# Kernel optimization log

Measured on AMD Instinct MI355X. Metric: run time of the kernel, lower is better.

## Reference

```python
import jax, jax.numpy as jnp
import numpy as np

# ---- forest structure (static) ----
B = 32                      # number of trees in the batch
DEPTH = 12                  # topological levels per tree
LEVELS = [2 ** d for d in range(DEPTH)]           # nodes per level (root=level 0)
STARTS = np.concatenate([[0], np.cumsum(LEVELS)[:-1]]).astype(int)
NPG = int(sum(LEVELS))      # 4095 nodes per graph, node 0 = root
N = B * NPG                 # 131040 total nodes
VOCAB = 20000               # dataset.PAD_TOKEN_VALUE + 1
PAD = VOCAB - 1             # padding_idx
E = 256                     # embedding_dim (x_size)
H = 256                     # lstm_output_dim (h_size)
C = 104                     # num_classes (extra_non_linear=None)


def setup_inputs() -> dict:
    key = jax.random.key(0)
    ks = jax.random.split(key, 8)
    # random parent in the previous level for every non-root node (irregular fan-in)
    rng = np.random.RandomState(0)
    par = np.full(N, -1, dtype=np.int64)
    for g in range(B):
        off = g * NPG
        for d in range(1, DEPTH):
            nd = LEVELS[d]
            par[off + STARTS[d]: off + STARTS[d] + nd] = (
                off + STARTS[d - 1] + rng.randint(0, LEVELS[d - 1], size=nd))
    s = 0.05
    return {
        'x': jax.random.randint(ks[0], (N,), 0, VOCAB),
        'par': jnp.asarray(par),
        'emb': jax.random.normal(ks[1], (VOCAB, E), jnp.float32) * s,
        'W_iou': jax.random.normal(ks[2], (3 * H, E), jnp.float32) * s,
        'U_iou': jax.random.normal(ks[3], (3 * H, H), jnp.float32) * s,
        'b_iou': jnp.zeros((1, 3 * H), jnp.float32),
        'U_f_w': jax.random.normal(ks[4], (H, H), jnp.float32) * s,
        'U_f_b': jnp.zeros((H,), jnp.float32),
        'lin_w': jax.random.normal(ks[5], (C, H), jnp.float32) * s,
        'lin_b': jnp.zeros((C,), jnp.float32),
    }


def _forward(x, par, emb, W_iou, U_iou, b_iou, U_f_w, U_f_b, lin_w, lin_b):
    emb = emb.at[PAD].set(0.0)                 # padding_idx row is zero
    x_vec = emb[x]                             # [N, E]
    iou = x_vec @ W_iou.T                      # [N, 3H], W_iou has no bias
    h = jnp.zeros((N, H), x_vec.dtype)
    c = jnp.zeros((N, H), x_vec.dtype)
    offs = jnp.arange(B) * NPG
    # topological propagation: leaves (deepest level) -> root, per generation
    for d in range(DEPTH - 1, -1, -1):
        nd = LEVELS[d]
        nids = (offs[:, None] + STARTS[d] + jnp.arange(nd)).reshape(-1)  # [B*nd]
        iou_n = iou[nids]
        if d < DEPTH - 1:
            nc = LEVELS[d + 1]
            cids = (offs[:, None] + STARTS[d + 1] + jnp.arange(nc)).reshape(-1)
            h_ch = h[cids]                     # mailbox gather of child states
            c_ch = c[cids]
            p = par[cids]                      # global parent id per child
            seg = (p // NPG) * nd + (p % NPG - STARTS[d])  # parent slot in this level
            f = jax.nn.sigmoid(h_ch @ U_f_w.T + U_f_b)     # per-child forget gate
            h_tild = jax.ops.segment_sum(h_ch, seg, num_segments=B * nd)
            c_agg = jax.ops.segment_sum(f * c_ch, seg, num_segments=B * nd)
            iou_n = iou_n + h_tild @ U_iou.T
            c_n = c_agg
        else:
            c_n = jnp.zeros((B * nd, H), x_vec.dtype)
        iou_n = iou_n + b_iou
        i, o, u = jnp.split(iou_n, 3, axis=1)
        c_new = jax.nn.sigmoid(i) * jnp.tanh(u) + c_n
        h_new = jax.nn.sigmoid(o) * jnp.tanh(c_new)
        h = h.at[nids].set(h_new)
        c = c.at[nids].set(c_new)
    roots = h[offs]                            # graph.ndata['h'][0] per graph
    return roots @ lin_w.T + lin_b             # [B, num_classes]


def reference(x, par, emb, W_iou, U_iou, b_iou, U_f_w, U_f_b, lin_w, lin_b):
    return _forward(x, par, emb, W_iou, U_iou, b_iou, U_f_w, U_f_b, lin_w, lin_b)
```

## Files before the change

### kernel.cpp

```cpp
#include <hip/hip_runtime.h>
#include <hip/hip_bf16.h>


#define B_G     32
#define NPG     4095
#define NTOT    (B_G * NPG)
#define NCLS    104
#define VOCAB   20000
#define PAD_TOK 19999
#define KCAP    24
#define LB(d)   (32 * ((1 << (d)) - 1))

#define EMB_BLKS  2500
#define WUC_BLKS  1536
#define UFC_BLKS  256
#define PREP_BLKS 512
#define CONV_BLKS (EMB_BLKS + WUC_BLKS + UFC_BLKS + PREP_BLKS)

typedef unsigned short u16;
typedef unsigned int   u32;
typedef __attribute__((ext_vector_type(8))) short bfrag8;
typedef __attribute__((ext_vector_type(4))) float ffrag4;

__device__ __forceinline__ float bf2f(u16 v) {
    union { u32 u; float f; } x; x.u = ((u32)v) << 16; return x.f;
}
__device__ __forceinline__ u16 f2bf(float f) {
    union { __hip_bfloat16 h; u16 u; } c; c.h = __float2bfloat16(f); return c.u;
}
__device__ __forceinline__ float loadv(const void* b, int i, int isf32) {
    return isf32 ? ((const float*)b)[i] : bf2f(((const u16*)b)[i]);
}
__device__ __forceinline__ float sigf(float x) { return 1.f / (1.f + __expf(-x)); }

__global__ __launch_bounds__(384) void probe_kernel(
    const void* emb, const void* Wiou, const void* Uiou,
    const void* Ufw, const void* lw,
    const int* x32, const int* par32, int* flags)
{
    if (blockIdx.x != 0) return;
    const int w = threadIdx.x >> 6, lane = threadIdx.x & 63;
    const void* ptrs[5] = { emb, Wiou, Uiou, Ufw, lw };
    if (w < 5) {
        const u16* p = (const u16*)ptrs[w];
        int big = 0;
        #pragma unroll
        for (int k = 0; k < 2; ++k) {
            u32 e = (((u32)p[lane * 2 + k]) << 16 >> 23) & 0xFF;
            if (e >= 129) ++big;
        }
        unsigned long long m1 = __ballot(big >= 1);
        unsigned long long m2 = __ballot(big >= 2);
        int tot = __popcll(m1) + __popcll(m2);
        if (lane == 0) flags[w] = (tot >= 4) ? 1 : 0;
    } else if (w == 5) {
        int bad = (lane < 8) ? (x32[2 * lane + 1] != 0) : 0;
        unsigned long long mx = __ballot(bad != 0);
        if (lane == 0) {
            flags[5] = (mx == 0) ? 1 : 0;
            flags[6] = (par32[3] == 0 && par32[5] == 0) ? 1 : 0;
        }
    }
}

__global__ __launch_bounds__(256) void convert_kernel(
    const void* __restrict__ emb, u16* __restrict__ embb,
    const void* __restrict__ Wiou, const void* __restrict__ Uiou,
    u16* __restrict__ wuc,
    const void* __restrict__ Ufw, u16* __restrict__ ufc,
    const int* __restrict__ x, const int* __restrict__ par,
    int* __restrict__ tokLvl, int* __restrict__ cnt, int* __restrict__ bucket,
    const int* __restrict__ flags)
{
    const int b = blockIdx.x;
    if (b < EMB_BLKS) {
        int i8 = (b * 256 + (int)threadIdx.x) * 8;
        if (i8 >= VOCAB * 256) return;
        u16 v[8];
        if ((i8 >> 8) == PAD_TOK) {
            #pragma unroll
            for (int s = 0; s < 8; ++s) v[s] = 0;
        } else if (flags[0]) {
            const float* e = (const float*)emb + i8;
            float4 a = *(const float4*)e;
            float4 c = *(const float4*)(e + 4);
            v[0]=f2bf(a.x); v[1]=f2bf(a.y); v[2]=f2bf(a.z); v[3]=f2bf(a.w);
            v[4]=f2bf(c.x); v[5]=f2bf(c.y); v[6]=f2bf(c.z); v[7]=f2bf(c.w);
        } else {
            *(uint4*)v = *(const uint4*)((const u16*)emb + i8);
        }
        *(uint4*)(embb + i8) = *(uint4*)v;
    } else if (b < EMB_BLKS + WUC_BLKS) {
        int idx = (b - EMB_BLKS) * 256 + (int)threadIdx.x;
        if (idx >= 16 * 768 * 32) return;
        int c   = idx / 24576;
        int rem = idx - c * 24576;
        int out = rem >> 5;
        int kk  = rem & 31;
        int k   = c * 32 + kk;
        float v = (k < 256) ? loadv(Wiou, out * 256 + k, flags[1])
                            : loadv(Uiou, out * 256 + (k - 256), flags[2]);
        wuc[idx] = f2bf(v);
    } else if (b < EMB_BLKS + WUC_BLKS + UFC_BLKS) {
        int idx = (b - EMB_BLKS - WUC_BLKS) * 256 + (int)threadIdx.x;
        if (idx >= 8 * 256 * 32) return;
        int c   = idx >> 13;
        int rem = idx & 8191;
        int out = rem >> 5;
        int kk  = rem & 31;
        ufc[idx] = f2bf(loadv(Ufw, out * 256 + c * 32 + kk, flags[3]));
    } else {
        int gid = (b - EMB_BLKS - WUC_BLKS - UFC_BLKS) * 256 + (int)threadIdx.x;
        if (gid >= NTOT) return;
        int g     = (int)((u32)gid / NPG);
        int local = gid - g * NPG;
        int v  = local + 1;
        int d  = 31 - __clz(v);
        int j  = local - ((1 << d) - 1);
        int tok = flags[5] ? x[2 * gid] : x[gid];
        if (tok < 0 || tok >= VOCAB) tok = PAD_TOK;
        tokLvl[LB(d) + (g << d) + j] = tok;
        if (local > 0) {
            int p  = flags[6] ? par[2 * gid] : par[gid];
            p = max(0, min(p, NTOT - 1));
            int pg = (int)((u32)p / NPG);
            int pl = p - pg * NPG;
            int pd = d - 1;
            int ps = LB(pd) + (pg << pd) + (pl - ((1 << pd) - 1));
            ps = max(0, min(ps, 65503));
            int slot = atomicAdd(&cnt[ps], 1);
            if (slot < KCAP) bucket[(size_t)ps * KCAP + slot] = (g << d) + j;
        }
    }
}

__global__ __launch_bounds__(256, 3) void gemm1_kernel(
    const u16* __restrict__ hch, u16* cbuf,
    const u16* __restrict__ ufc, const void* __restrict__ ufb,
    const int* __restrict__ flags)
{
    __shared__ union {
        struct { u16 As[64][40]; u16 Bs[256][40]; } k;
        u16 tile[64][264];
    } sm;
    auto& As = sm.k.As;
    auto& Bs = sm.k.Bs;
    auto& tile = sm.tile;
    const int t = threadIdx.x;
    const int w = t >> 6, lane = t & 63, quad = lane >> 4, l15 = lane & 15;
    const int m0 = blockIdx.x * 64;
    const int f_uf = flags[3];

    ffrag4 acc[4][4];
    #pragma unroll
    for (int i = 0; i < 4; ++i)
        #pragma unroll
        for (int j = 0; j < 4; ++j) acc[i][j] = (ffrag4)0.f;

    const int arow = t >> 2, aseg = t & 3;
    for (int c = 0; c < 8; ++c) {
        *(uint4*)&As[arow][aseg * 8] =
            *(const uint4*)(hch + (size_t)(m0 + arow) * 256 + c * 32 + aseg * 8);
        #pragma unroll
        for (int r16 = 0; r16 < 4; ++r16) {
            int row = r16 * 64 + arow;
            *(uint4*)&Bs[row][aseg * 8] =
                *(const uint4*)(ufc + ((size_t)c * 256 + row) * 32 + aseg * 8);
        }
        __syncthreads();
        bfrag8 a[4], b[4];
        #pragma unroll
        for (int mt = 0; mt < 4; ++mt) a[mt] = *(bfrag8*)&As[mt * 16 + l15][quad * 8];
        #pragma unroll
        for (int nt = 0; nt < 4; ++nt) b[nt] = *(bfrag8*)&Bs[w * 64 + nt * 16 + l15][quad * 8];
        #pragma unroll
        for (int mt = 0; mt < 4; ++mt)
            #pragma unroll
            for (int nt = 0; nt < 4; ++nt)
                acc[mt][nt] = __builtin_amdgcn_mfma_f32_16x16x32_bf16(a[mt], b[nt], acc[mt][nt], 0, 0, 0);
        __syncthreads();
    }

    const int srow = t >> 2, sseg = t & 3;
    const size_t sgb = (size_t)(m0 + srow) * 256 + sseg * 64;
    #pragma unroll
    for (int k = 0; k < 8; ++k)
        *(uint4*)&tile[srow][sseg * 64 + k * 8] = *(const uint4*)(cbuf + sgb + k * 8);
    __syncthreads();

    #pragma unroll
    for (int nt = 0; nt < 4; ++nt) {
        int hu = w * 64 + nt * 16 + l15;
        float fb = loadv(ufb, hu, f_uf);
        #pragma unroll
        for (int mt = 0; mt < 4; ++mt) {
            #pragma unroll
            for (int r = 0; r < 4; ++r) {
                int row = mt * 16 + quad * 4 + r;
                float f = sigf(acc[mt][nt][r] + fb);
                tile[row][hu] = f2bf(f * bf2f(tile[row][hu]));
            }
        }
    }
    __syncthreads();
    #pragma unroll
    for (int k = 0; k < 8; ++k)
        *(uint4*)(cbuf + sgb + k * 8) = *(const uint4*)&tile[srow][sseg * 64 + k * 8];
}

__global__ __launch_bounds__(256) void agg_kernel(
    int NN, const u32* __restrict__ hch32, const u32* __restrict__ fcch32,
    const int* __restrict__ cnt_d, const int* __restrict__ bucket_d,
    u32* __restrict__ htild32, u32* __restrict__ cagg32)
{
    int pi  = blockIdx.x * 2 + (threadIdx.x >> 7);
    int col = threadIdx.x & 127;
    if (pi >= NN) return;
    int nc = min(cnt_d[pi], KCAP);
    float h0 = 0.f, h1 = 0.f, c0 = 0.f, c1 = 0.f;
    for (int ci = 0; ci < nc; ++ci) {
        int ch = bucket_d[(size_t)pi * KCAP + ci];
        u32 hv = hch32[(size_t)ch * 128 + col];
        u32 fv = fcch32[(size_t)ch * 128 + col];
        h0 += bf2f((u16)(hv & 0xffff)); h1 += bf2f((u16)(hv >> 16));
        c0 += bf2f((u16)(fv & 0xffff)); c1 += bf2f((u16)(fv >> 16));
    }
    htild32[(size_t)pi * 128 + col] = (u32)f2bf(h0) | ((u32)f2bf(h1) << 16);
    cagg32[(size_t)pi * 128 + col]  = (u32)f2bf(c0) | ((u32)f2bf(c1) << 16);
}

__global__ __launch_bounds__(256, 3) void gemm2_kernel(
    int nchunk, int NN,
    const int* __restrict__ tokLvl_d, const u16* __restrict__ embb,
    const u16* __restrict__ wuc, const void* __restrict__ biou,
    const u16* __restrict__ htild, const u16* __restrict__ cagg,
    u16* __restrict__ hdst, u16* __restrict__ cdst,
    const int* __restrict__ flags)
{
    __shared__ union {
        struct { u16 As[128][40]; u16 Bs[192][40]; } k;
        u16 tile[128][72];
    } sm;
    __shared__ int toks[128];
    auto& As = sm.k.As;
    auto& Bs = sm.k.Bs;
    auto& tile = sm.tile;
    const int t = threadIdx.x;
    const int w = t >> 6, lane = t & 63, quad = lane >> 4, l15 = lane & 15;
    const int m0 = blockIdx.x * 128;
    const int q  = blockIdx.y;
    const int f_b = flags[1];

    if (t < 128) toks[t] = tokLvl_d[m0 + t];
    __syncthreads();

    ffrag4 acc[8][3];
    #pragma unroll
    for (int i = 0; i < 8; ++i)
        #pragma unroll
        for (int j = 0; j < 3; ++j) acc[i][j] = (ffrag4)0.f;

    const int arow = t >> 1, ac0 = (t & 1) * 16;
    const int brow = t >> 2, bseg = t & 3;
    for (int c = 0; c < nchunk; ++c) {
        if (c < 8) {
            const u16* e = embb + (size_t)toks[arow] * 256 + c * 32 + ac0;
            *(uint4*)&As[arow][ac0]     = *(const uint4*)e;
            *(uint4*)&As[arow][ac0 + 8] = *(const uint4*)(e + 8);
        } else {
            const u16* hsrc = htild + (size_t)(m0 + arow) * 256 + (c - 8) * 32 + ac0;
            *(uint4*)&As[arow][ac0]     = *(const uint4*)hsrc;
            *(uint4*)&As[arow][ac0 + 8] = *(const uint4*)(hsrc + 8);
        }
        #pragma unroll
        for (int g = 0; g < 3; ++g) {
            *(uint4*)&Bs[g * 64 + brow][bseg * 8] =
                *(const uint4*)(wuc + ((size_t)c * 768 + g * 256 + q * 64 + brow) * 32 + bseg * 8);
        }
        __syncthreads();
        bfrag8 a[8], b[3];
        #pragma unroll
        for (int mt = 0; mt < 8; ++mt) a[mt] = *(bfrag8*)&As[mt * 16 + l15][quad * 8];
        #pragma unroll
        for (int g = 0; g < 3; ++g) b[g] = *(bfrag8*)&Bs[g * 64 + w * 16 + l15][quad * 8];
        #pragma unroll
        for (int mt = 0; mt < 8; ++mt)
            #pragma unroll
            for (int g = 0; g < 3; ++g)
                acc[mt][g] = __builtin_amdgcn_mfma_f32_16x16x32_bf16(a[mt], b[g], acc[mt][g], 0, 0, 0);
        __syncthreads();
    }

    const int hu  = q * 64 + w * 16 + l15;
    const int huL = w * 16 + l15;
    const float bi = loadv(biou, hu,       f_b);
    const float bo = loadv(biou, 256 + hu, f_b);
    const float bu = loadv(biou, 512 + hu, f_b);

    const int srow = t >> 1, sseg = t & 1;
    const size_t sgbase = (size_t)(m0 + srow) * 256 + q * 64 + sseg * 32;
    const bool svalid = (m0 + srow) < NN;

    if (cagg) {
        if (svalid) {
            #pragma unroll
            for (int k = 0; k < 4; ++k)
                *(uint4*)&tile[srow][sseg * 32 + k * 8] =
                    *(const uint4*)(cagg + sgbase + k * 8);
        }
    }
    __syncthreads();

    u16 cnv[8][4];
    #pragma unroll
    for (int mt = 0; mt < 8; ++mt) {
        #pragma unroll
        for (int r = 0; r < 4; ++r) {
            int row = mt * 16 + quad * 4 + r;
            float cg = cagg ? bf2f(tile[row][huL]) : 0.f;
            float iv = acc[mt][0][r] + bi;
            float ov = acc[mt][1][r] + bo;
            float uv = acc[mt][2][r] + bu;
            float cn = sigf(iv) * tanhf(uv) + cg;
            float hn = sigf(ov) * tanhf(cn);
            cnv[mt][r] = f2bf(cn);
            tile[row][huL] = f2bf(hn);
        }
    }
    __syncthreads();
    if (svalid) {
        #pragma unroll
        for (int k = 0; k < 4; ++k)
            *(uint4*)(hdst + sgbase + k * 8) = *(const uint4*)&tile[srow][sseg * 32 + k * 8];
    }
    __syncthreads();
    #pragma unroll
    for (int mt = 0; mt < 8; ++mt)
        #pragma unroll
        for (int r = 0; r < 4; ++r)
            tile[mt * 16 + quad * 4 + r][huL] = cnv[mt][r];
    __syncthreads();
    if (svalid) {
        #pragma unroll
        for (int k = 0; k < 4; ++k)
            *(uint4*)(cdst + sgbase + k * 8) = *(const uint4*)&tile[srow][sseg * 32 + k * 8];
    }
}

__global__ __launch_bounds__(1024, 1) void tail_kernel(
    const int* __restrict__ tokLvl, const u16* __restrict__ embb,
    const u16* __restrict__ wuc, const void* __restrict__ biou,
    const u16* __restrict__ ufc, const void* __restrict__ ufb,
    const u16* __restrict__ hB, const u16* __restrict__ cB,
    const int* __restrict__ cnt, const int* __restrict__ bucket,
    const void* __restrict__ lw, const void* __restrict__ lb,
    float* __restrict__ out, const int* __restrict__ flags)
{
    __shared__ u16 hs[64][264];
    __shared__ u16 cs[64][264];
    __shared__ u16 hts[32][264];
    __shared__ u16 cts[32][264];
    __shared__ float lred[8][NCLS];
    const int t = threadIdx.x;
    const int g = blockIdx.x;
    const int w = t >> 6;
    const int lane = t & 63, quad = lane >> 4, l15 = lane & 15;
    const int f_uf = flags[3], f_b = flags[1], f_lw = flags[4];

    #pragma unroll 1
    for (int i = t; i < 64 * 32; i += 1024) {
        int j = i >> 5, seg = i & 31;
        size_t off = (((size_t)((g << 6) + j)) << 8) + seg * 8;
        *(uint4*)&hs[j][seg * 8] = *(const uint4*)(hB + off);
        *(uint4*)&cs[j][seg * 8] = *(const uint4*)(cB + off);
    }
    __syncthreads();

    #pragma unroll 1
    for (int d = 5; d >= 0; --d) {
        const int ncr = 1 << (d + 1);
        const int np  = 1 << d;
        const int lvb = LB(d) + (g << d);
        const int hu  = w * 16 + l15;

        {
            ffrag4 facc[4];
            #pragma unroll
            for (int i = 0; i < 4; ++i) facc[i] = (ffrag4)0.f;
            #pragma unroll 4
            for (int c = 0; c < 8; ++c) {
                bfrag8 a[4];
                #pragma unroll
                for (int mt = 0; mt < 4; ++mt)
                    a[mt] = *(const bfrag8*)&hs[mt * 16 + l15][c * 32 + quad * 8];
                bfrag8 b = *(const bfrag8*)(ufc + ((size_t)c * 256 + w * 16 + l15) * 32 + quad * 8);
                #pragma unroll
                for (int mt = 0; mt < 4; ++mt)
                    facc[mt] = __builtin_amdgcn_mfma_f32_16x16x32_bf16(a[mt], b, facc[mt], 0, 0, 0);
            }
            float fb = loadv(ufb, hu, f_uf);
            #pragma unroll
            for (int mt = 0; mt < 4; ++mt) {
                #pragma unroll
                for (int r = 0; r < 4; ++r) {
                    int j = mt * 16 + quad * 4 + r;
                    if (j < ncr) {
                        float f = sigf(facc[mt][r] + fb);
                        cs[j][hu] = f2bf(f * bf2f(cs[j][hu]));
                    }
                }
            }
        }

        {
            const int pr = lane >> 3;
            const int colb = (w * 8 + (lane & 7)) * 2;
            #pragma unroll 1
            for (int pi = pr; pi < np; pi += 8) {
                int nc = min(cnt[lvb + pi], KCAP);
                const int* bk = bucket + (size_t)(lvb + pi) * KCAP;
                float h0 = 0.f, h1 = 0.f, c0 = 0.f, c1 = 0.f;
                #pragma unroll 1
                for (int ci = 0; ci < nc; ++ci) {
                    int j = bk[ci] & (ncr - 1);
                    u32 hv = *(const u32*)&hs[j][colb];
                    u32 cv = *(const u32*)&cs[j][colb];
                    h0 += bf2f((u16)(hv & 0xffff)); h1 += bf2f((u16)(hv >> 16));
                    c0 += bf2f((u16)(cv & 0xffff)); c1 += bf2f((u16)(cv >> 16));
                }
                *(u32*)&hts[pi][colb] = (u32)f2bf(h0) | ((u32)f2bf(h1) << 16);
                *(u32*)&cts[pi][colb] = (u32)f2bf(c0) | ((u32)f2bf(c1) << 16);
            }
        }
        __syncthreads();

        {
            int tok0 = tokLvl[lvb + min(l15, np - 1)];
            int tok1 = tokLvl[lvb + min(16 + l15, np - 1)];
            const u16* wb = wuc + ((size_t)w * 16 + l15) * 32 + quad * 8;
            ffrag4 acc[2][3];
            #pragma unroll
            for (int i = 0; i < 2; ++i)
                #pragma unroll
                for (int j = 0; j < 3; ++j) acc[i][j] = (ffrag4)0.f;
            #pragma unroll 4
            for (int c = 0; c < 8; ++c) {
                bfrag8 a0 = *(const bfrag8*)(embb + (size_t)tok0 * 256 + c * 32 + quad * 8);
                bfrag8 a1 = *(const bfrag8*)(embb + (size_t)tok1 * 256 + c * 32 + quad * 8);
                #pragma unroll
                for (int g3 = 0; g3 < 3; ++g3) {
                    bfrag8 b = *(const bfrag8*)(wb + ((size_t)c * 768 + g3 * 256) * 32);
                    acc[0][g3] = __builtin_amdgcn_mfma_f32_16x16x32_bf16(a0, b, acc[0][g3], 0, 0, 0);
                    acc[1][g3] = __builtin_amdgcn_mfma_f32_16x16x32_bf16(a1, b, acc[1][g3], 0, 0, 0);
                }
            }
            #pragma unroll 4
            for (int c8 = 0; c8 < 8; ++c8) {
                bfrag8 a0 = *(const bfrag8*)&hts[l15][c8 * 32 + quad * 8];
                bfrag8 a1 = *(const bfrag8*)&hts[16 + l15][c8 * 32 + quad * 8];
                #pragma unroll
                for (int g3 = 0; g3 < 3; ++g3) {
                    bfrag8 b = *(const bfrag8*)(wb + ((size_t)(c8 + 8) * 768 + g3 * 256) * 32);
                    acc[0][g3] = __builtin_amdgcn_mfma_f32_16x16x32_bf16(a0, b, acc[0][g3], 0, 0, 0);
                    acc[1][g3] = __builtin_amdgcn_mfma_f32_16x16x32_bf16(a1, b, acc[1][g3], 0, 0, 0);
                }
            }
            float bi = loadv(biou, hu,       f_b);
            float bo = loadv(biou, 256 + hu, f_b);
            float bu = loadv(biou, 512 + hu, f_b);
            #pragma unroll
            for (int mt = 0; mt < 2; ++mt) {
                #pragma unroll
                for (int r = 0; r < 4; ++r) {
                    int p = mt * 16 + quad * 4 + r;
                    if (p < np) {
                        float iv = acc[mt][0][r] + bi;
                        float ov = acc[mt][1][r] + bo;
                        float uv = acc[mt][2][r] + bu;
                        float cn = sigf(iv) * tanhf(uv) + bf2f(cts[p][hu]);
                        float hn = sigf(ov) * tanhf(cn);
                        hs[p][hu] = f2bf(hn);
                        cs[p][hu] = f2bf(cn);
                    }
                }
            }
        }
        __syncthreads();
    }

    {
        const int o  = t & 127;
        const int ks = t >> 7;
        if (o < NCLS) {
            float acc = 0.f;
            #pragma unroll 8
            for (int k = ks * 32; k < ks * 32 + 32; ++k)
                acc += loadv(lw, o * 256 + k, f_lw) * bf2f(hs[0][k]);
            lred[ks][o] = acc;
        }
        __syncthreads();
        if (t < NCLS) {
            float s = 0.f;
            #pragma unroll
            for (int i = 0; i < 8; ++i) s += lred[i][t];
            out[(size_t)g * NCLS + t] = s + loadv(lb, t, f_lw);
        }
    }
}

__global__ void fill_kernel(float* out, int n, float v) {
    int i = blockIdx.x * 256 + threadIdx.x;
    if (i < n) out[i] = v;
}

extern "C" void kernel_launch(void* const* d_in, const int* in_sizes, int n_in,
                              void* d_out, int out_size, void* d_ws, size_t ws_size,
                              hipStream_t stream)
{
    float* out = (float*)d_out;

    static const int exp_sizes[10] = {131040, 131040, 5120000, 196608, 196608,
                                      768, 65536, 256, 26624, 104};
    bool shapes_ok = (n_in == 10) && (out_size == B_G * NCLS);
    for (int i = 0; i < 10 && shapes_ok; ++i)
        if (in_sizes[i] != exp_sizes[i]) shapes_ok = false;
    if (!shapes_ok) {
        fill_kernel<<<(out_size + 255) / 256, 256, 0, stream>>>(out, out_size, 2.0f);
        return;
    }

    const int* x     = (const int*)d_in[0];
    const int* par   = (const int*)d_in[1];
    const void* emb  = d_in[2];
    const void* Wiou = d_in[3];
    const void* Uiou = d_in[4];
    const void* biou = d_in[5];
    const void* Ufw  = d_in[6];
    const void* Ufb  = d_in[7];
    const void* lw   = d_in[8];
    const void* lb   = d_in[9];

    char* W = (char*)d_ws;
    u16* hA     = (u16*)(W + 0);
    u16* hB     = (u16*)(W + 33554432);
    u16* cA     = (u16*)(W + 50331648);
    u16* cB     = (u16*)(W + 83886080);
    u16* htild  = (u16*)(W + 100663296);
    u16* cagg   = (u16*)(W + 117440512);
    u16* WUc    = (u16*)(W + 134217728);
    u16* Ufc    = (u16*)(W + 135004160);
    int* tokLvl = (int*)(W + 135135232);
    int* cnt    = (int*)(W + 135659520);
    int* bucket = (int*)(W + 135921664);
    u16* embb   = (u16*)(W + 142213120);
    int* flags  = (int*)(W + 152453120);
    const size_t NEED = 152453184;
    if (ws_size < NEED) {
        fill_kernel<<<(out_size + 255) / 256, 256, 0, stream>>>(out, out_size, 1.0f);
        return;
    }

    hipMemsetAsync(cnt, 0, 65536 * sizeof(int), stream);
    probe_kernel<<<1, 384, 0, stream>>>(emb, Wiou, Uiou, Ufw, lw, x, par, flags);
    convert_kernel<<<CONV_BLKS, 256, 0, stream>>>(
        emb, embb, Wiou, Uiou, WUc, Ufw, Ufc,
        x, par, tokLvl, cnt, bucket, flags);

    gemm2_kernel<<<dim3(512, 4), 256, 0, stream>>>(
        8, 65536, tokLvl + LB(11), embb, WUc, biou,
        nullptr, nullptr, hA, cA, flags);

    for (int d = 10; d >= 6; --d) {
        const int cl = d + 1;
        const int NC = B_G << cl;
        const int NN = B_G << d;
        const u16* hch = (cl & 1) ? hA : hB;
        u16*       cch = (cl & 1) ? cA : cB;
        u16* hdst = (d & 1) ? hA : hB;
        u16* cdst = (d & 1) ? cA : cB;
        gemm1_kernel<<<NC / 64, 256, 0, stream>>>(hch, cch, Ufc, Ufb, flags);
        agg_kernel<<<(NN + 1) / 2, 256, 0, stream>>>(
            NN, (const u32*)hch, (const u32*)cch,
            cnt + LB(d), bucket + (size_t)LB(d) * KCAP,
            (u32*)htild, (u32*)cagg);
        gemm2_kernel<<<dim3((NN + 127) / 128, 4), 256, 0, stream>>>(
            16, NN, tokLvl + LB(d), embb, WUc, biou,
            htild, cagg, hdst, cdst, flags);
    }

    tail_kernel<<<B_G, 1024, 0, stream>>>(
        tokLvl, embb, WUc, biou, Ufc, Ufb,
        hB, cB, cnt, bucket, lw, lb, out, flags);
}
```

Baseline: 625.4 us.

## Register-prefetch next K-chunk in GEMM kernels and stage tail metadata in LDS

The two tiled MFMA kernels (forget-gate and iou) now load the next K chunk of A and B into registers while the current chunk's MFMAs run, then write them to LDS after the barrier. This overlaps global loads with compute. The tail kernel preloads per-level counts, tokens and child buckets into shared memory once and hoists the bias loads out of the level loop. Its inner MFMA loops are fully unrolled two chunks at a time to expose more load parallelism. The cost is higher register pressure and extra LDS use.

```diff
diff --git a/kernel.cpp b/kernel.cpp
--- a/kernel.cpp
+++ b/kernel.cpp
@@ -158,16 +158,26 @@
         for (int j = 0; j < 4; ++j) acc[i][j] = (ffrag4)0.f;
 
     const int arow = t >> 2, aseg = t & 3;
+
+    *(uint4*)&As[arow][aseg * 8] =
+        *(const uint4*)(hch + (size_t)(m0 + arow) * 256 + aseg * 8);
+    #pragma unroll
+    for (int r16 = 0; r16 < 4; ++r16)
+        *(uint4*)&Bs[r16 * 64 + arow][aseg * 8] =
+            *(const uint4*)(ufc + ((size_t)r16 * 64 + arow) * 32 + aseg * 8);
+    __syncthreads();
+
     for (int c = 0; c < 8; ++c) {
-        *(uint4*)&As[arow][aseg * 8] =
-            *(const uint4*)(hch + (size_t)(m0 + arow) * 256 + c * 32 + aseg * 8);
-        #pragma unroll
-        for (int r16 = 0; r16 < 4; ++r16) {
-            int row = r16 * 64 + arow;
-            *(uint4*)&Bs[row][aseg * 8] =
-                *(const uint4*)(ufc + ((size_t)c * 256 + row) * 32 + aseg * 8);
-        }
-        __syncthreads();
+        const bool more = (c + 1 < 8);
+        uint4 ra, rb0, rb1, rb2, rb3;
+        if (more) {
+            const int cn = c + 1;
+            ra  = *(const uint4*)(hch + (size_t)(m0 + arow) * 256 + cn * 32 + aseg * 8);
+            rb0 = *(const uint4*)(ufc + ((size_t)cn * 256 +   0 + arow) * 32 + aseg * 8);
+            rb1 = *(const uint4*)(ufc + ((size_t)cn * 256 +  64 + arow) * 32 + aseg * 8);
+            rb2 = *(const uint4*)(ufc + ((size_t)cn * 256 + 128 + arow) * 32 + aseg * 8);
+            rb3 = *(const uint4*)(ufc + ((size_t)cn * 256 + 192 + arow) * 32 + aseg * 8);
+        }
         bfrag8 a[4], b[4];
         #pragma unroll
         for (int mt = 0; mt < 4; ++mt) a[mt] = *(bfrag8*)&As[mt * 16 + l15][quad * 8];
@@ -179,6 +189,14 @@
             for (int nt = 0; nt < 4; ++nt)
                 acc[mt][nt] = __builtin_amdgcn_mfma_f32_16x16x32_bf16(a[mt], b[nt], acc[mt][nt], 0, 0, 0);
         __syncthreads();
+        if (more) {
+            *(uint4*)&As[arow][aseg * 8] = ra;
+            *(uint4*)&Bs[  0 + arow][aseg * 8] = rb0;
+            *(uint4*)&Bs[ 64 + arow][aseg * 8] = rb1;
+            *(uint4*)&Bs[128 + arow][aseg * 8] = rb2;
+            *(uint4*)&Bs[192 + arow][aseg * 8] = rb3;
+            __syncthreads();
+        }
     }
 
     const int srow = t >> 2, sseg = t & 3;
@@ -262,22 +280,33 @@
 
     const int arow = t >> 1, ac0 = (t & 1) * 16;
     const int brow = t >> 2, bseg = t & 3;
+
+    {
+        const u16* e = embb + (size_t)toks[arow] * 256 + ac0;
+        *(uint4*)&As[arow][ac0]     = *(const uint4*)e;
+        *(uint4*)&As[arow][ac0 + 8] = *(const uint4*)(e + 8);
+        #pragma unroll
+        for (int g = 0; g < 3; ++g)
+            *(uint4*)&Bs[g * 64 + brow][bseg * 8] =
+                *(const uint4*)(wuc + ((size_t)g * 256 + q * 64 + brow) * 32 + bseg * 8);
+    }
+    __syncthreads();
+
     for (int c = 0; c < nchunk; ++c) {
-        if (c < 8) {
-            const u16* e = embb + (size_t)toks[arow] * 256 + c * 32 + ac0;
-            *(uint4*)&As[arow][ac0]     = *(const uint4*)e;
-            *(uint4*)&As[arow][ac0 + 8] = *(const uint4*)(e + 8);
-        } else {
-            const u16* hsrc = htild + (size_t)(m0 + arow) * 256 + (c - 8) * 32 + ac0;
-            *(uint4*)&As[arow][ac0]     = *(const uint4*)hsrc;
-            *(uint4*)&As[arow][ac0 + 8] = *(const uint4*)(hsrc + 8);
-        }
-        #pragma unroll
-        for (int g = 0; g < 3; ++g) {
-            *(uint4*)&Bs[g * 64 + brow][bseg * 8] =
-                *(const uint4*)(wuc + ((size_t)c * 768 + g * 256 + q * 64 + brow) * 32 + bseg * 8);
-        }
-        __syncthreads();
+        const bool more = (c + 1 < nchunk);
+        uint4 ra0, ra1, rb0, rb1, rb2;
+        if (more) {
+            const int cn = c + 1;
+            const u16* asrc = (cn < 8)
+                ? embb  + (size_t)toks[arow] * 256 + cn * 32 + ac0
+                : htild + (size_t)(m0 + arow) * 256 + (cn - 8) * 32 + ac0;
+            ra0 = *(const uint4*)asrc;
+            ra1 = *(const uint4*)(asrc + 8);
+            const u16* bsrc = wuc + ((size_t)cn * 768 + q * 64 + brow) * 32 + bseg * 8;
+            rb0 = *(const uint4*)bsrc;
+            rb1 = *(const uint4*)(bsrc + (size_t)256 * 32);
+            rb2 = *(const uint4*)(bsrc + (size_t)512 * 32);
+        }
         bfrag8 a[8], b[3];
         #pragma unroll
         for (int mt = 0; mt < 8; ++mt) a[mt] = *(bfrag8*)&As[mt * 16 + l15][quad * 8];
@@ -289,6 +318,14 @@
             for (int g = 0; g < 3; ++g)
                 acc[mt][g] = __builtin_amdgcn_mfma_f32_16x16x32_bf16(a[mt], b[g], acc[mt][g], 0, 0, 0);
         __syncthreads();
+        if (more) {
+            *(uint4*)&As[arow][ac0]     = ra0;
+            *(uint4*)&As[arow][ac0 + 8] = ra1;
+            *(uint4*)&Bs[  0 + brow][bseg * 8] = rb0;
+            *(uint4*)&Bs[ 64 + brow][bseg * 8] = rb1;
+            *(uint4*)&Bs[128 + brow][bseg * 8] = rb2;
+            __syncthreads();
+        }
     }
 
     const int hu  = q * 64 + w * 16 + l15;
@@ -361,11 +398,20 @@
     __shared__ u16 hts[32][264];
     __shared__ u16 cts[32][264];
     __shared__ float lred[8][NCLS];
+    __shared__ int cntS[64];
+    __shared__ int toksS[64];
+    __shared__ int bucketS[64][KCAP];
     const int t = threadIdx.x;
     const int g = blockIdx.x;
     const int w = t >> 6;
     const int lane = t & 63, quad = lane >> 4, l15 = lane & 15;
     const int f_uf = flags[3], f_b = flags[1], f_lw = flags[4];
+    const int hu = w * 16 + l15;
+
+    const float fbv = loadv(ufb, hu, f_uf);
+    const float biv = loadv(biou, hu,       f_b);
+    const float bov = loadv(biou, 256 + hu, f_b);
+    const float buv = loadv(biou, 512 + hu, f_b);
 
     #pragma unroll 1
     for (int i = t; i < 64 * 32; i += 1024) {
@@ -374,38 +420,58 @@
         *(uint4*)&hs[j][seg * 8] = *(const uint4*)(hB + off);
         *(uint4*)&cs[j][seg * 8] = *(const uint4*)(cB + off);
     }
+    #pragma unroll 1
+    for (int d5 = 5; d5 >= 0; --d5) {
+        const int np5  = 1 << d5;
+        const int sb5  = 64 - (2 << d5);
+        const int lvb5 = LB(d5) + (g << d5);
+        #pragma unroll 1
+        for (int i = t; i < np5 * (KCAP + 1); i += 1024) {
+            int pi = i / (KCAP + 1), f = i - pi * (KCAP + 1);
+            if (f == 0) {
+                cntS[sb5 + pi]  = cnt[lvb5 + pi];
+                toksS[sb5 + pi] = tokLvl[lvb5 + pi];
+            } else {
+                bucketS[sb5 + pi][f - 1] = bucket[(size_t)(lvb5 + pi) * KCAP + f - 1];
+            }
+        }
+    }
     __syncthreads();
 
     #pragma unroll 1
     for (int d = 5; d >= 0; --d) {
         const int ncr = 1 << (d + 1);
         const int np  = 1 << d;
-        const int lvb = LB(d) + (g << d);
-        const int hu  = w * 16 + l15;
+        const int sb  = 64 - (2 << d);
 
         {
             ffrag4 facc[4];
             #pragma unroll
             for (int i = 0; i < 4; ++i) facc[i] = (ffrag4)0.f;
-            #pragma unroll 4
-            for (int c = 0; c < 8; ++c) {
-                bfrag8 a[4];
-                #pragma unroll
-                for (int mt = 0; mt < 4; ++mt)
-                    a[mt] = *(const bfrag8*)&hs[mt * 16 + l15][c * 32 + quad * 8];
-                bfrag8 b = *(const bfrag8*)(ufc + ((size_t)c * 256 + w * 16 + l15) * 32 + quad * 8);
-                #pragma unroll
-                for (int mt = 0; mt < 4; ++mt)
-                    facc[mt] = __builtin_amdgcn_mfma_f32_16x16x32_bf16(a[mt], b, facc[mt], 0, 0, 0);
-            }
-            float fb = loadv(ufb, hu, f_uf);
+            const u16* ub = ufc + ((size_t)w * 16 + l15) * 32 + quad * 8;
+            #pragma unroll
+            for (int c = 0; c < 8; c += 2) {
+                bfrag8 b0 = *(const bfrag8*)(ub + (size_t)c * 8192);
+                bfrag8 b1 = *(const bfrag8*)(ub + (size_t)(c + 1) * 8192);
+                bfrag8 a0[4], a1[4];
+                #pragma unroll
+                for (int mt = 0; mt < 4; ++mt) {
+                    a0[mt] = *(const bfrag8*)&hs[mt * 16 + l15][c * 32 + quad * 8];
+                    a1[mt] = *(const bfrag8*)&hs[mt * 16 + l15][(c + 1) * 32 + quad * 8];
+                }
+                #pragma unroll
+                for (int mt = 0; mt < 4; ++mt) {
+                    facc[mt] = __builtin_amdgcn_mfma_f32_16x16x32_bf16(a0[mt], b0, facc[mt], 0, 0, 0);
+                    facc[mt] = __builtin_amdgcn_mfma_f32_16x16x32_bf16(a1[mt], b1, facc[mt], 0, 0, 0);
+                }
+            }
             #pragma unroll
             for (int mt = 0; mt < 4; ++mt) {
                 #pragma unroll
                 for (int r = 0; r < 4; ++r) {
                     int j = mt * 16 + quad * 4 + r;
                     if (j < ncr) {
-                        float f = sigf(facc[mt][r] + fb);
+                        float f = sigf(facc[mt][r] + fbv);
                         cs[j][hu] = f2bf(f * bf2f(cs[j][hu]));
                     }
                 }
@@ -417,12 +483,11 @@
             const int colb = (w * 8 + (lane & 7)) * 2;
             #pragma unroll 1
             for (int pi = pr; pi < np; pi += 8) {
-                int nc = min(cnt[lvb + pi], KCAP);
-                const int* bk = bucket + (size_t)(lvb + pi) * KCAP;
+                int nc = min(cntS[sb + pi], KCAP);
                 float h0 = 0.f, h1 = 0.f, c0 = 0.f, c1 = 0.f;
                 #pragma unroll 1
                 for (int ci = 0; ci < nc; ++ci) {
-                    int j = bk[ci] & (ncr - 1);
+                    int j = bucketS[sb + pi][ci] & (ncr - 1);
                     u32 hv = *(const u32*)&hs[j][colb];
                     u32 cv = *(const u32*)&cs[j][colb];
                     h0 += bf2f((u16)(hv & 0xffff)); h1 += bf2f((u16)(hv >> 16));
@@ -435,48 +500,65 @@
         __syncthreads();
 
         {
-            int tok0 = tokLvl[lvb + min(l15, np - 1)];
-            int tok1 = tokLvl[lvb + min(16 + l15, np - 1)];
+            int tok0 = toksS[sb + min(l15, np - 1)];
+            int tok1 = toksS[sb + min(16 + l15, np - 1)];
             const u16* wb = wuc + ((size_t)w * 16 + l15) * 32 + quad * 8;
+            const u16* e0 = embb + (size_t)tok0 * 256 + quad * 8;
+            const u16* e1 = embb + (size_t)tok1 * 256 + quad * 8;
             ffrag4 acc[2][3];
             #pragma unroll
             for (int i = 0; i < 2; ++i)
                 #pragma unroll
                 for (int j = 0; j < 3; ++j) acc[i][j] = (ffrag4)0.f;
-            #pragma unroll 4
-            for (int c = 0; c < 8; ++c) {
-                bfrag8 a0 = *(const bfrag8*)(embb + (size_t)tok0 * 256 + c * 32 + quad * 8);
-                bfrag8 a1 = *(const bfrag8*)(embb + (size_t)tok1 * 256 + c * 32 + quad * 8);
+            #pragma unroll
+            for (int c = 0; c < 8; c += 2) {
+                bfrag8 a00 = *(const bfrag8*)(e0 + c * 32);
+                bfrag8 a10 = *(const bfrag8*)(e1 + c * 32);
+                bfrag8 a01 = *(const bfrag8*)(e0 + (c + 1) * 32);
+                bfrag8 a11 = *(const bfrag8*)(e1 + (c + 1) * 32);
+                bfrag8 b0[3], b1[3];
                 #pragma unroll
                 for (int g3 = 0; g3 < 3; ++g3) {
-                    bfrag8 b = *(const bfrag8*)(wb + ((size_t)c * 768 + g3 * 256) * 32);
-                    acc[0][g3] = __builtin_amdgcn_mfma_f32_16x16x32_bf16(a0, b, acc[0][g3], 0, 0, 0);
-                    acc[1][g3] = __builtin_amdgcn_mfma_f32_16x16x32_bf16(a1, b, acc[1][g3], 0, 0, 0);
-                }
-            }
-            #pragma unroll 4
-            for (int c8 = 0; c8 < 8; ++c8) {
-                bfrag8 a0 = *(const bfrag8*)&hts[l15][c8 * 32 + quad * 8];
-                bfrag8 a1 = *(const bfrag8*)&hts[16 + l15][c8 * 32 + quad * 8];
+                    b0[g3] = *(const bfrag8*)(wb + ((size_t)c * 768 + g3 * 256) * 32);
+                    b1[g3] = *(const bfrag8*)(wb + ((size_t)(c + 1) * 768 + g3 * 256) * 32);
+                }
                 #pragma unroll
                 for (int g3 = 0; g3 < 3; ++g3) {
-                    bfrag8 b = *(const bfrag8*)(wb + ((size_t)(c8 + 8) * 768 + g3 * 256) * 32);
-                    acc[0][g3] = __builtin_amdgcn_mfma_f32_16x16x32_bf16(a0, b, acc[0][g3], 0, 0, 0);
-                    acc[1][g3] = __builtin_amdgcn_mfma_f32_16x16x32_bf16(a1, b, acc[1][g3], 0, 0, 0);
-                }
-            }
-            float bi = loadv(biou, hu,       f_b);
-            float bo = loadv(biou, 256 + hu, f_b);
-            float bu = loadv(biou, 512 + hu, f_b);
+                    acc[0][g3] = __builtin_amdgcn_mfma_f32_16x16x32_bf16(a00, b0[g3], acc[0][g3], 0, 0, 0);
+                    acc[1][g3] = __builtin_amdgcn_mfma_f32_16x16x32_bf16(a10, b0[g3], acc[1][g3], 0, 0, 0);
+                    acc[0][g3] = __builtin_amdgcn_mfma_f32_16x16x32_bf16(a01, b1[g3], acc[0][g3], 0, 0, 0);
+                    acc[1][g3] = __builtin_amdgcn_mfma_f32_16x16x32_bf16(a11, b1[g3], acc[1][g3], 0, 0, 0);
+                }
+            }
+            #pragma unroll
+            for (int c8 = 0; c8 < 8; c8 += 2) {
+                bfrag8 a00 = *(const bfrag8*)&hts[l15][c8 * 32 + quad * 8];
+                bfrag8 a10 = *(const bfrag8*)&hts[16 + l15][c8 * 32 + quad * 8];
+                bfrag8 a01 = *(const bfrag8*)&hts[l15][(c8 + 1) * 32 + quad * 8];
+                bfrag8 a11 = *(const bfrag8*)&hts[16 + l15][(c8 + 1) * 32 + quad * 8];
+                bfrag8 b0[3], b1[3];
+                #pragma unroll
+                for (int g3 = 0; g3 < 3; ++g3) {
+                    b0[g3] = *(const bfrag8*)(wb + ((size_t)(c8 + 8) * 768 + g3 * 256) * 32);
+                    b1[g3] = *(const bfrag8*)(wb + ((size_t)(c8 + 9) * 768 + g3 * 256) * 32);
+                }
+                #pragma unroll
+                for (int g3 = 0; g3 < 3; ++g3) {
+                    acc[0][g3] = __builtin_amdgcn_mfma_f32_16x16x32_bf16(a00, b0[g3], acc[0][g3], 0, 0, 0);
+                    acc[1][g3] = __builtin_amdgcn_mfma_f32_16x16x32_bf16(a10, b0[g3], acc[1][g3], 0, 0, 0);
+                    acc[0][g3] = __builtin_amdgcn_mfma_f32_16x16x32_bf16(a01, b1[g3], acc[0][g3], 0, 0, 0);
+                    acc[1][g3] = __builtin_amdgcn_mfma_f32_16x16x32_bf16(a11, b1[g3], acc[1][g3], 0, 0, 0);
+                }
+            }
             #pragma unroll
             for (int mt = 0; mt < 2; ++mt) {
                 #pragma unroll
                 for (int r = 0; r < 4; ++r) {
                     int p = mt * 16 + quad * 4 + r;
                     if (p < np) {
-                        float iv = acc[mt][0][r] + bi;
-                        float ov = acc[mt][1][r] + bo;
-                        float uv = acc[mt][2][r] + bu;
+                        float iv = acc[mt][0][r] + biv;
+                        float ov = acc[mt][1][r] + bov;
+                        float uv = acc[mt][2][r] + buv;
                         float cn = sigf(iv) * tanhf(uv) + bf2f(cts[p][hu]);
                         float hn = sigf(ov) * tanhf(cn);
                         hs[p][hu] = f2bf(hn);
```

Measured after the change: 673.4 us. 7.7% more time.
